# Kernel optimization log

Hardware: AMD Instinct MI355X
Metric: run time of the kernel (lower is better)

## Reference

```python
import jax, jax.numpy as jnp
import numpy as np

GROUP_SIZE = 128
TOP_K = 2
ZERO_POINT = 8  # Marlin symmetric zero point: w = scale * (q - 8)


def _dequant_int4(q, scales, group_size):
    # q: [E, N, K] int values in [0,15]; scales: [E, N, K//group_size]
    s = jnp.repeat(scales, group_size, axis=-1)  # [E, N, K]
    return (q.astype(jnp.float32) - float(ZERO_POINT)) * s


def setup_inputs() -> dict:
    key = jax.random.key(0)
    k1, k2, k3, k4, k5, k6 = jax.random.split(key, 6)
    B, S, H, I, E = 2, 1024, 2048, 1408, 8
    router_logits = jax.random.normal(k1, (B, S, E), dtype=jnp.float32)
    hidden_states = jax.random.normal(k2, (B, S, H), dtype=jnp.float32)
    fc_gate_up_qweights = jax.random.randint(k3, (E, 2 * I, H), 0, 16, dtype=jnp.int32)
    fc_gate_up_scales = jax.random.uniform(k4, (E, 2 * I, H // GROUP_SIZE), dtype=jnp.float32) * 0.02
    fc_down_qweights = jax.random.randint(k5, (E, H, I), 0, 16, dtype=jnp.int32)
    fc_down_scales = jax.random.uniform(k6, (E, H, I // GROUP_SIZE), dtype=jnp.float32) * 0.02
    return {
        "router_logits": router_logits,
        "hidden_states": hidden_states,
        "fc_gate_up_qweights": fc_gate_up_qweights,
        "fc_gate_up_scales": fc_gate_up_scales,
        "fc_down_qweights": fc_down_qweights,
        "fc_down_scales": fc_down_scales,
    }


def reference(router_logits, hidden_states, fc_gate_up_qweights, fc_gate_up_scales,
              fc_down_qweights, fc_down_scales):
    B, S, H = hidden_states.shape
    E = router_logits.shape[-1]
    T = B * S
    x = hidden_states.reshape(T, H)
    logits = router_logits.reshape(T, E)

    # top-k routing with softmax over selected logits
    top_vals, top_idx = jax.lax.top_k(logits, TOP_K)          # [T, k]
    top_w = jax.nn.softmax(top_vals, axis=-1)                 # [T, k]
    route_w = jnp.zeros((T, E), x.dtype).at[jnp.arange(T)[:, None], top_idx].set(top_w)  # [T, E]

    # dequantize int4 weights: scale * (q - 8), per-group along K
    w_gate_up = _dequant_int4(fc_gate_up_qweights, fc_gate_up_scales, GROUP_SIZE)  # [E, 2I, H]
    w_down = _dequant_int4(fc_down_qweights, fc_down_scales, GROUP_SIZE)          # [E, H, I]

    # grouped GEMM (dense over experts, masked by routing weights)
    gu = jnp.einsum('th,enh->ten', x, w_gate_up)              # [T, E, 2I]
    gate, up = jnp.split(gu, 2, axis=-1)
    act = jax.nn.silu(gate) * up                              # SwiGLU, [T, E, I]
    out = jnp.einsum('tei,ehi,te->th', act, w_down, route_w)  # [T, H]
    return out.reshape(B, S, H)
```

## Files before the change

### kernel.cpp

```cpp
#include <hip/hip_runtime.h>
#include <hip/hip_bf16.h>

#define T_TOKENS 2048
#define H_DIM    2048
#define I_DIM    1408
#define E_NUM    8

typedef __bf16 bf16;
typedef __attribute__((ext_vector_type(8))) __bf16  bf16x8;
typedef __attribute__((ext_vector_type(4))) float   floatx4;

static const size_t OFF_COUNTS = 0;
static const size_t OFF_LISTS  = 256;
static const size_t OFF_WLISTS = OFF_LISTS + (size_t)T_TOKENS * E_NUM * 4;
static const size_t OFF_XB     = 131328;
static const size_t OFF_ACT    = OFF_XB + (size_t)T_TOKENS * H_DIM * 2;
static const size_t OFF_GUPK   = OFF_ACT + (size_t)2 * T_TOKENS * I_DIM * 2;
static const size_t OFF_DNPK   = OFF_GUPK + (size_t)E_NUM * 22 * 32 * 16384;
static const size_t OFF_TMP    = OFF_GUPK;

__global__ __launch_bounds__(256) void pack_gu_kernel(const int* __restrict__ q,
                                                      const float* __restrict__ sc,
                                                      bf16* __restrict__ out)
{
    const int b = blockIdx.x;
    const int t = threadIdx.x;
    const int e = b / 2816;
    const int grow = b - e * 2816;
    const int4* qp = reinterpret_cast<const int4*>(q + (size_t)b * H_DIM) + t * 2;
    int4 a = qp[0], c = qp[1];
    float s = sc[(size_t)b * 16 + (t >> 4)];
    float m8s = -8.f * s;
    bf16x8 bv;
    bv[0] = (bf16)fmaf((float)a.x, s, m8s);
    bv[1] = (bf16)fmaf((float)a.y, s, m8s);
    bv[2] = (bf16)fmaf((float)a.z, s, m8s);
    bv[3] = (bf16)fmaf((float)a.w, s, m8s);
    bv[4] = (bf16)fmaf((float)c.x, s, m8s);
    bv[5] = (bf16)fmaf((float)c.y, s, m8s);
    bv[6] = (bf16)fmaf((float)c.z, s, m8s);
    bv[7] = (bf16)fmaf((float)c.w, s, m8s);
    const int is_up = grow >= I_DIM;
    const int icol  = grow - (is_up ? I_DIM : 0);
    const int nt    = icol >> 6;
    const int r     = ((((icol >> 4) & 3) * 2 + is_up) * 16) + (icol & 15);
    size_t dst = ((((size_t)e * 22 + nt) * 32 + (t >> 3)) * 128 + r) * 8 + ((t & 7) ^ (r & 7));
    reinterpret_cast<bf16x8*>(out)[dst] = bv;
}

__global__ __launch_bounds__(256) void pack_dn_kernel(const int* __restrict__ q,
                                                      const float* __restrict__ sc,
                                                      bf16* __restrict__ out)
{
    const int b = blockIdx.x;
    const int t = threadIdx.x;
    if (t >= 176) return;
    const int e = b >> 11;
    const int grow = b & 2047;
    const int4* qp = reinterpret_cast<const int4*>(q + (size_t)b * I_DIM) + t * 2;
    int4 a = qp[0], c = qp[1];
    float s = sc[(size_t)b * 11 + (t >> 4)];
    float m8s = -8.f * s;
    bf16x8 bv;
    bv[0] = (bf16)fmaf((float)a.x, s, m8s);
    bv[1] = (bf16)fmaf((float)a.y, s, m8s);
    bv[2] = (bf16)fmaf((float)a.z, s, m8s);
    bv[3] = (bf16)fmaf((float)a.w, s, m8s);
    bv[4] = (bf16)fmaf((float)c.x, s, m8s);
    bv[5] = (bf16)fmaf((float)c.y, s, m8s);
    bv[6] = (bf16)fmaf((float)c.z, s, m8s);
    bv[7] = (bf16)fmaf((float)c.w, s, m8s);
    const int nt = grow >> 7;
    const int r  = grow & 127;
    size_t dst = ((((size_t)e * 16 + nt) * 22 + (t >> 3)) * 128 + r) * 8 + ((t & 7) ^ (r & 7));
    reinterpret_cast<bf16x8*>(out)[dst] = bv;
}

__global__ void xconv_kernel(const float* __restrict__ x, bf16* __restrict__ xb)
{
    int i = blockIdx.x * blockDim.x + threadIdx.x;
    const float4* x4 = reinterpret_cast<const float4*>(x) + (size_t)i * 2;
    float4 v0 = x4[0], v1 = x4[1];
    bf16x8 bv;
    bv[0] = (bf16)v0.x; bv[1] = (bf16)v0.y; bv[2] = (bf16)v0.z; bv[3] = (bf16)v0.w;
    bv[4] = (bf16)v1.x; bv[5] = (bf16)v1.y; bv[6] = (bf16)v1.z; bv[7] = (bf16)v1.w;
    *reinterpret_cast<bf16x8*>(xb + (size_t)i * 8) = bv;
}

__global__ void router_kernel(const float* __restrict__ logits,
                              int* __restrict__ counts,
                              int* __restrict__ lists,
                              float* __restrict__ wlists)
{
    int t = blockIdx.x * blockDim.x + threadIdx.x;
    if (t >= T_TOKENS) return;
    const float* l = logits + (size_t)t * E_NUM;
    float v0 = -1e30f, v1 = -1e30f;
    int i0 = 0, i1 = 0;
    #pragma unroll
    for (int e = 0; e < E_NUM; ++e) {
        float v = l[e];
        if (v > v0) { v1 = v0; i1 = i0; v0 = v; i0 = e; }
        else if (v > v1) { v1 = v; i1 = e; }
    }
    float w0 = 1.f / (1.f + __expf(v1 - v0));
    float w1 = 1.f - w0;
    int p0 = atomicAdd(&counts[i0], 1);
    lists[i0 * T_TOKENS + p0] = t * 2 + 0;
    wlists[i0 * T_TOKENS + p0] = w0;
    int p1 = atomicAdd(&counts[i1], 1);
    lists[i1 * T_TOKENS + p1] = t * 2 + 1;
    wlists[i1 * T_TOKENS + p1] = w1;
}

__global__ __launch_bounds__(256) void gemm1_kernel(
    const bf16* __restrict__ xb,
    const bf16* __restrict__ wpk,
    const int*  __restrict__ counts,
    const int*  __restrict__ lists,
    bf16*       __restrict__ act)
{
    const int e   = blockIdx.z;
    const int cnt = counts[e];
    const int m0  = blockIdx.y * 128;
    if (m0 >= cnt) return;
    const int nt  = blockIdx.x;

    __shared__ __align__(16) bf16 Al[8192];
    __shared__ __align__(16) bf16 Bl[8192];
    __shared__ int meta[128];

    const int tid = threadIdx.x;
    if (tid < 128) {
        int m = m0 + tid;
        meta[tid] = lists[e * T_TOKENS + (m < cnt ? m : 0)];
    }
    __syncthreads();

    const int lane = tid & 63;
    const int wv = tid >> 6;
    const int wm = wv >> 1, wn = wv & 1;

    int    aoff[4];
    size_t agbl[4];
    #pragma unroll
    for (int j = 0; j < 4; ++j) {
        int g = tid + 256 * j;
        int arow = g >> 3, cg = g & 7;
        aoff[j] = arow * 64 + ((cg ^ (arow & 7)) * 8);
        agbl[j] = (size_t)(meta[arow] >> 1) * H_DIM + cg * 8;
    }
    const bf16* bt = wpk + ((size_t)e * 22 + nt) * (32 * 8192) + tid * 8;

    int afr[2][4], bfr[2][4];
    #pragma unroll
    for (int ks = 0; ks < 2; ++ks) {
        int gidx = ks * 4 + (lane >> 4);
        #pragma unroll
        for (int t4 = 0; t4 < 4; ++t4) {
            int ra = wm * 64 + t4 * 16 + (lane & 15);
            afr[ks][t4] = ra * 64 + ((gidx ^ (ra & 7)) * 8);
            int rb = wn * 64 + t4 * 16 + (lane & 15);
            bfr[ks][t4] = rb * 64 + ((gidx ^ (rb & 7)) * 8);
        }
    }

    floatx4 acc[4][4];
    #pragma unroll
    for (int i = 0; i < 4; ++i)
        #pragma unroll
        for (int j = 0; j < 4; ++j)
            acc[i][j] = (floatx4){0.f, 0.f, 0.f, 0.f};

    for (int k0 = 0; k0 < H_DIM; k0 += 64) {
        #pragma unroll
        for (int j = 0; j < 4; ++j) {
            bf16x8 v = *reinterpret_cast<const bf16x8*>(xb + agbl[j] + k0);
            *reinterpret_cast<bf16x8*>(&Al[aoff[j]]) = v;
        }
        const bf16* bsrc = bt + (size_t)(k0 >> 6) * 8192;
        #pragma unroll
        for (int j = 0; j < 4; ++j) {
            bf16x8 v = *reinterpret_cast<const bf16x8*>(bsrc + j * 2048);
            *reinterpret_cast<bf16x8*>(&Bl[tid * 8 + j * 2048]) = v;
        }
        __syncthreads();
        #pragma unroll
        for (int ks = 0; ks < 2; ++ks) {
            bf16x8 af[4], bff[4];
            #pragma unroll
            for (int mt = 0; mt < 4; ++mt)
                af[mt] = *reinterpret_cast<const bf16x8*>(&Al[afr[ks][mt]]);
            #pragma unroll
            for (int ntf = 0; ntf < 4; ++ntf)
                bff[ntf] = *reinterpret_cast<const bf16x8*>(&Bl[bfr[ks][ntf]]);
            #pragma unroll
            for (int mt = 0; mt < 4; ++mt)
                #pragma unroll
                for (int ntf = 0; ntf < 4; ++ntf)
                    acc[mt][ntf] = __builtin_amdgcn_mfma_f32_16x16x32_bf16(af[mt], bff[ntf], acc[mt][ntf], 0, 0, 0);
        }
        __syncthreads();
    }

    const int rbase = (lane >> 4) * 4;
    const int cn = lane & 15;
    #pragma unroll
    for (int mt = 0; mt < 4; ++mt) {
        #pragma unroll
        for (int j = 0; j < 2; ++j) {
            floatx4 g = acc[mt][2 * j];
            floatx4 u = acc[mt][2 * j + 1];
            int col = nt * 64 + (wn * 2 + j) * 16 + cn;
            #pragma unroll
            for (int r = 0; r < 4; ++r) {
                int lrow = wm * 64 + mt * 16 + rbase + r;
                if (m0 + lrow < cnt) {
                    float gate = g[r], up = u[r];
                    float a = gate / (1.f + __expf(-gate)) * up;
                    act[(size_t)meta[lrow] * I_DIM + col] = (bf16)a;
                }
            }
        }
    }
}

__global__ __launch_bounds__(256) void gemm2_kernel(
    const bf16*  __restrict__ act,
    const bf16*  __restrict__ wpk,
    const int*   __restrict__ counts,
    const int*   __restrict__ lists,
    const float* __restrict__ wlists,
    float*       __restrict__ tmp)
{
    const int e   = blockIdx.z;
    const int cnt = counts[e];
    const int m0  = blockIdx.y * 128;
    if (m0 >= cnt) return;
    const int nt  = blockIdx.x;

    __shared__ __align__(16) bf16 Al[8192];
    __shared__ __align__(16) bf16 Bl[8192];
    __shared__ int   meta[128];
    __shared__ float wmeta[128];

    const int tid = threadIdx.x;
    if (tid < 128) {
        int m = m0 + tid;
        int mm = (m < cnt) ? m : 0;
        meta[tid]  = lists[e * T_TOKENS + mm];
        wmeta[tid] = wlists[e * T_TOKENS + mm];
    }
    __syncthreads();

    const int lane = tid & 63;
    const int wv = tid >> 6;
    const int wm = wv >> 1, wn = wv & 1;

    int    aoff[4];
    size_t agbl[4];
    #pragma unroll
    for (int j = 0; j < 4; ++j) {
        int g = tid + 256 * j;
        int arow = g >> 3, cg = g & 7;
        aoff[j] = arow * 64 + ((cg ^ (arow & 7)) * 8);
        agbl[j] = (size_t)meta[arow] * I_DIM + cg * 8;
    }
    const bf16* bt = wpk + ((size_t)e * 16 + nt) * (22 * 8192) + tid * 8;

    int afr[2][4], bfr[2][4];
    #pragma unroll
    for (int ks = 0; ks < 2; ++ks) {
        int gidx = ks * 4 + (lane >> 4);
        #pragma unroll
        for (int t4 = 0; t4 < 4; ++t4) {
            int ra = wm * 64 + t4 * 16 + (lane & 15);
            afr[ks][t4] = ra * 64 + ((gidx ^ (ra & 7)) * 8);
            int rb = wn * 64 + t4 * 16 + (lane & 15);
            bfr[ks][t4] = rb * 64 + ((gidx ^ (rb & 7)) * 8);
        }
    }

    floatx4 acc[4][4];
    #pragma unroll
    for (int i = 0; i < 4; ++i)
        #pragma unroll
        for (int j = 0; j < 4; ++j)
            acc[i][j] = (floatx4){0.f, 0.f, 0.f, 0.f};

    for (int kt = 0; kt < 22; ++kt) {
        #pragma unroll
        for (int j = 0; j < 4; ++j) {
            bf16x8 v = *reinterpret_cast<const bf16x8*>(act + agbl[j] + kt * 64);
            *reinterpret_cast<bf16x8*>(&Al[aoff[j]]) = v;
        }
        const bf16* bsrc = bt + (size_t)kt * 8192;
        #pragma unroll
        for (int j = 0; j < 4; ++j) {
            bf16x8 v = *reinterpret_cast<const bf16x8*>(bsrc + j * 2048);
            *reinterpret_cast<bf16x8*>(&Bl[tid * 8 + j * 2048]) = v;
        }
        __syncthreads();
        #pragma unroll
        for (int ks = 0; ks < 2; ++ks) {
            bf16x8 af[4], bff[4];
            #pragma unroll
            for (int mt = 0; mt < 4; ++mt)
                af[mt] = *reinterpret_cast<const bf16x8*>(&Al[afr[ks][mt]]);
            #pragma unroll
            for (int ntf = 0; ntf < 4; ++ntf)
                bff[ntf] = *reinterpret_cast<const bf16x8*>(&Bl[bfr[ks][ntf]]);
            #pragma unroll
            for (int mt = 0; mt < 4; ++mt)
                #pragma unroll
                for (int ntf = 0; ntf < 4; ++ntf)
                    acc[mt][ntf] = __builtin_amdgcn_mfma_f32_16x16x32_bf16(af[mt], bff[ntf], acc[mt][ntf], 0, 0, 0);
        }
        __syncthreads();
    }

    const int rbase = (lane >> 4) * 4;
    const int cn = lane & 15;
    #pragma unroll
    for (int mt = 0; mt < 4; ++mt) {
        #pragma unroll
        for (int ntf = 0; ntf < 4; ++ntf) {
            floatx4 v = acc[mt][ntf];
            int col = nt * 128 + wn * 64 + ntf * 16 + cn;
            #pragma unroll
            for (int r = 0; r < 4; ++r) {
                int lrow = wm * 64 + mt * 16 + rbase + r;
                if (m0 + lrow < cnt) {
                    tmp[(size_t)meta[lrow] * H_DIM + col] = wmeta[lrow] * v[r];
                }
            }
        }
    }
}

__global__ void finalize_kernel(const float* __restrict__ tmp, float* __restrict__ out)
{
    int i4 = blockIdx.x * blockDim.x + threadIdx.x;
    int t  = i4 >> 9;
    int h  = (i4 & 511) * 4;
    float4 a = *reinterpret_cast<const float4*>(tmp + ((size_t)2 * t) * H_DIM + h);
    float4 b = *reinterpret_cast<const float4*>(tmp + ((size_t)(2 * t + 1)) * H_DIM + h);
    float4 o;
    o.x = a.x + b.x; o.y = a.y + b.y; o.z = a.z + b.z; o.w = a.w + b.w;
    *reinterpret_cast<float4*>(out + (size_t)t * H_DIM + h) = o;
}

extern "C" void kernel_launch(void* const* d_in, const int* in_sizes, int n_in,
                              void* d_out, int out_size, void* d_ws, size_t ws_size,
                              hipStream_t stream)
{
    const float* router_logits = (const float*)d_in[0];
    const float* x             = (const float*)d_in[1];
    const int*   gu_q          = (const int*)d_in[2];
    const float* gu_s          = (const float*)d_in[3];
    const int*   dn_q          = (const int*)d_in[4];
    const float* dn_s          = (const float*)d_in[5];
    float* out = (float*)d_out;

    char* ws = (char*)d_ws;
    int*   counts = (int*)(ws + OFF_COUNTS);
    int*   lists  = (int*)(ws + OFF_LISTS);
    float* wlists = (float*)(ws + OFF_WLISTS);
    bf16*  xb     = (bf16*)(ws + OFF_XB);
    bf16*  act    = (bf16*)(ws + OFF_ACT);
    bf16*  gu_pk  = (bf16*)(ws + OFF_GUPK);
    bf16*  dn_pk  = (bf16*)(ws + OFF_DNPK);
    float* tmp    = (float*)(ws + OFF_TMP);

    hipMemsetAsync(counts, 0, E_NUM * sizeof(int), stream);

    pack_gu_kernel<<<E_NUM * 2816, 256, 0, stream>>>(gu_q, gu_s, gu_pk);
    pack_dn_kernel<<<E_NUM * 2048, 256, 0, stream>>>(dn_q, dn_s, dn_pk);
    xconv_kernel<<<T_TOKENS * H_DIM / 8 / 256, 256, 0, stream>>>(x, xb);
    router_kernel<<<T_TOKENS / 256, 256, 0, stream>>>(router_logits, counts, lists, wlists);

    gemm1_kernel<<<dim3(22, 16, 8), 256, 0, stream>>>(xb, gu_pk, counts, lists, act);
    gemm2_kernel<<<dim3(16, 16, 8), 256, 0, stream>>>(act, dn_pk, counts, lists, wlists, tmp);
    finalize_kernel<<<4096, 256, 0, stream>>>(tmp, out);
}
```

Measured before the change: 523.4 us.

## Use direct global-to-LDS loads, XCD-aware block remap, and atomic output accumulation

```diff
diff --git a/kernel.cpp b/kernel.cpp
--- a/kernel.cpp
+++ b/kernel.cpp
@@ -17,7 +17,13 @@
 static const size_t OFF_ACT    = OFF_XB + (size_t)T_TOKENS * H_DIM * 2;
 static const size_t OFF_GUPK   = OFF_ACT + (size_t)2 * T_TOKENS * I_DIM * 2;
 static const size_t OFF_DNPK   = OFF_GUPK + (size_t)E_NUM * 22 * 32 * 16384;
-static const size_t OFF_TMP    = OFF_GUPK;
+
+__device__ __forceinline__ void gload_lds16(const bf16* g, bf16* l)
+{
+    __builtin_amdgcn_global_load_lds((const __attribute__((address_space(1))) void*)g,
+                                     (__attribute__((address_space(3))) void*)l,
+                                     16, 0, 0);
+}
 
 __global__ __launch_bounds__(256) void pack_gu_kernel(const int* __restrict__ q,
                                                       const float* __restrict__ sc,
@@ -120,11 +126,13 @@
     const int*  __restrict__ lists,
     bf16*       __restrict__ act)
 {
-    const int e   = blockIdx.z;
+    const int lid = (blockIdx.x & 7) * 352 + (blockIdx.x >> 3);
+    const int e   = lid / 352;
+    const int r_  = lid - e * 352;
+    const int nt  = r_ >> 4;
+    const int m0  = (r_ & 15) * 128;
     const int cnt = counts[e];
-    const int m0  = blockIdx.y * 128;
     if (m0 >= cnt) return;
-    const int nt  = blockIdx.x;
 
     __shared__ __align__(16) bf16 Al[8192];
     __shared__ __align__(16) bf16 Bl[8192];
@@ -141,14 +149,12 @@
     const int wv = tid >> 6;
     const int wm = wv >> 1, wn = wv & 1;
 
-    int    aoff[4];
     size_t agbl[4];
     #pragma unroll
     for (int j = 0; j < 4; ++j) {
         int g = tid + 256 * j;
         int arow = g >> 3, cg = g & 7;
-        aoff[j] = arow * 64 + ((cg ^ (arow & 7)) * 8);
-        agbl[j] = (size_t)(meta[arow] >> 1) * H_DIM + cg * 8;
+        agbl[j] = (size_t)(meta[arow] >> 1) * H_DIM + ((cg ^ (arow & 7)) * 8);
     }
     const bf16* bt = wpk + ((size_t)e * 22 + nt) * (32 * 8192) + tid * 8;
 
@@ -174,16 +180,12 @@
 
     for (int k0 = 0; k0 < H_DIM; k0 += 64) {
         #pragma unroll
-        for (int j = 0; j < 4; ++j) {
-            bf16x8 v = *reinterpret_cast<const bf16x8*>(xb + agbl[j] + k0);
-            *reinterpret_cast<bf16x8*>(&Al[aoff[j]]) = v;
-        }
+        for (int j = 0; j < 4; ++j)
+            gload_lds16(xb + agbl[j] + k0, &Al[(tid + 256 * j) * 8]);
         const bf16* bsrc = bt + (size_t)(k0 >> 6) * 8192;
         #pragma unroll
-        for (int j = 0; j < 4; ++j) {
-            bf16x8 v = *reinterpret_cast<const bf16x8*>(bsrc + j * 2048);
-            *reinterpret_cast<bf16x8*>(&Bl[tid * 8 + j * 2048]) = v;
-        }
+        for (int j = 0; j < 4; ++j)
+            gload_lds16(bsrc + j * 2048, &Bl[tid * 8 + j * 2048]);
         __syncthreads();
         #pragma unroll
         for (int ks = 0; ks < 2; ++ks) {
@@ -231,13 +233,15 @@
     const int*   __restrict__ counts,
     const int*   __restrict__ lists,
     const float* __restrict__ wlists,
-    float*       __restrict__ tmp)
-{
-    const int e   = blockIdx.z;
+    float*       __restrict__ out)
+{
+    const int lid = (blockIdx.x & 7) * 256 + (blockIdx.x >> 3);
+    const int e   = lid >> 8;
+    const int r_  = lid & 255;
+    const int nt  = r_ >> 4;
+    const int m0  = (r_ & 15) * 128;
     const int cnt = counts[e];
-    const int m0  = blockIdx.y * 128;
     if (m0 >= cnt) return;
-    const int nt  = blockIdx.x;
 
     __shared__ __align__(16) bf16 Al[8192];
     __shared__ __align__(16) bf16 Bl[8192];
@@ -257,14 +261,12 @@
     const int wv = tid >> 6;
     const int wm = wv >> 1, wn = wv & 1;
 
-    int    aoff[4];
     size_t agbl[4];
     #pragma unroll
     for (int j = 0; j < 4; ++j) {
         int g = tid + 256 * j;
         int arow = g >> 3, cg = g & 7;
-        aoff[j] = arow * 64 + ((cg ^ (arow & 7)) * 8);
-        agbl[j] = (size_t)meta[arow] * I_DIM + cg * 8;
+        agbl[j] = (size_t)meta[arow] * I_DIM + ((cg ^ (arow & 7)) * 8);
     }
     const bf16* bt = wpk + ((size_t)e * 16 + nt) * (22 * 8192) + tid * 8;
 
@@ -290,16 +292,12 @@
 
     for (int kt = 0; kt < 22; ++kt) {
         #pragma unroll
-        for (int j = 0; j < 4; ++j) {
-            bf16x8 v = *reinterpret_cast<const bf16x8*>(act + agbl[j] + kt * 64);
-            *reinterpret_cast<bf16x8*>(&Al[aoff[j]]) = v;
-        }
+        for (int j = 0; j < 4; ++j)
+            gload_lds16(act + agbl[j] + kt * 64, &Al[(tid + 256 * j) * 8]);
         const bf16* bsrc = bt + (size_t)kt * 8192;
         #pragma unroll
-        for (int j = 0; j < 4; ++j) {
-            bf16x8 v = *reinterpret_cast<const bf16x8*>(bsrc + j * 2048);
-            *reinterpret_cast<bf16x8*>(&Bl[tid * 8 + j * 2048]) = v;
-        }
+        for (int j = 0; j < 4; ++j)
+            gload_lds16(bsrc + j * 2048, &Bl[tid * 8 + j * 2048]);
         __syncthreads();
         #pragma unroll
         for (int ks = 0; ks < 2; ++ks) {
@@ -331,23 +329,12 @@
             for (int r = 0; r < 4; ++r) {
                 int lrow = wm * 64 + mt * 16 + rbase + r;
                 if (m0 + lrow < cnt) {
-                    tmp[(size_t)meta[lrow] * H_DIM + col] = wmeta[lrow] * v[r];
+                    int tok = meta[lrow] >> 1;
+                    atomicAdd(&out[(size_t)tok * H_DIM + col], wmeta[lrow] * v[r]);
                 }
             }
         }
     }
-}
-
-__global__ void finalize_kernel(const float* __restrict__ tmp, float* __restrict__ out)
-{
-    int i4 = blockIdx.x * blockDim.x + threadIdx.x;
-    int t  = i4 >> 9;
-    int h  = (i4 & 511) * 4;
-    float4 a = *reinterpret_cast<const float4*>(tmp + ((size_t)2 * t) * H_DIM + h);
-    float4 b = *reinterpret_cast<const float4*>(tmp + ((size_t)(2 * t + 1)) * H_DIM + h);
-    float4 o;
-    o.x = a.x + b.x; o.y = a.y + b.y; o.z = a.z + b.z; o.w = a.w + b.w;
-    *reinterpret_cast<float4*>(out + (size_t)t * H_DIM + h) = o;
 }
 
 extern "C" void kernel_launch(void* const* d_in, const int* in_sizes, int n_in,
@@ -370,16 +357,15 @@
     bf16*  act    = (bf16*)(ws + OFF_ACT);
     bf16*  gu_pk  = (bf16*)(ws + OFF_GUPK);
     bf16*  dn_pk  = (bf16*)(ws + OFF_DNPK);
-    float* tmp    = (float*)(ws + OFF_TMP);
 
     hipMemsetAsync(counts, 0, E_NUM * sizeof(int), stream);
+    hipMemsetAsync(out, 0, (size_t)T_TOKENS * H_DIM * sizeof(float), stream);
 
     pack_gu_kernel<<<E_NUM * 2816, 256, 0, stream>>>(gu_q, gu_s, gu_pk);
     pack_dn_kernel<<<E_NUM * 2048, 256, 0, stream>>>(dn_q, dn_s, dn_pk);
     xconv_kernel<<<T_TOKENS * H_DIM / 8 / 256, 256, 0, stream>>>(x, xb);
     router_kernel<<<T_TOKENS / 256, 256, 0, stream>>>(router_logits, counts, lists, wlists);
 
-    gemm1_kernel<<<dim3(22, 16, 8), 256, 0, stream>>>(xb, gu_pk, counts, lists, act);
-    gemm2_kernel<<<dim3(16, 16, 8), 256, 0, stream>>>(act, dn_pk, counts, lists, wlists, tmp);
-    finalize_kernel<<<4096, 256, 0, stream>>>(tmp, out);
-}
+    gemm1_kernel<<<22 * 16 * E_NUM, 256, 0, stream>>>(xb, gu_pk, counts, lists, act);
+    gemm2_kernel<<<16 * 16 * E_NUM, 256, 0, stream>>>(act, dn_pk, counts, lists, wlists, out);
+}
```

Result: slower. 544.4 us (+4.0%).

## Use 256x256 tiles with double-buffered direct global-to-LDS loads in MoE GEMMs

Applied to the files above, without the earlier changes.

```diff
diff --git a/kernel.cpp b/kernel.cpp
--- a/kernel.cpp
+++ b/kernel.cpp
@@ -9,6 +9,8 @@
 typedef __bf16 bf16;
 typedef __attribute__((ext_vector_type(8))) __bf16  bf16x8;
 typedef __attribute__((ext_vector_type(4))) float   floatx4;
+
+#define MFMA __builtin_amdgcn_mfma_f32_16x16x32_bf16
 
 static const size_t OFF_COUNTS = 0;
 static const size_t OFF_LISTS  = 256;
@@ -16,8 +18,15 @@
 static const size_t OFF_XB     = 131328;
 static const size_t OFF_ACT    = OFF_XB + (size_t)T_TOKENS * H_DIM * 2;
 static const size_t OFF_GUPK   = OFF_ACT + (size_t)2 * T_TOKENS * I_DIM * 2;
-static const size_t OFF_DNPK   = OFF_GUPK + (size_t)E_NUM * 22 * 32 * 16384;
+static const size_t OFF_DNPK   = OFF_GUPK + (size_t)E_NUM * 11 * 32 * 32768;
 static const size_t OFF_TMP    = OFF_GUPK;
+
+__device__ __forceinline__ void gload_lds16(const bf16* g, bf16* l)
+{
+    __builtin_amdgcn_global_load_lds((const __attribute__((address_space(1))) void*)g,
+                                     (__attribute__((address_space(3))) void*)l,
+                                     16, 0, 0);
+}
 
 __global__ __launch_bounds__(256) void pack_gu_kernel(const int* __restrict__ q,
                                                       const float* __restrict__ sc,
@@ -42,9 +51,9 @@
     bv[7] = (bf16)fmaf((float)c.w, s, m8s);
     const int is_up = grow >= I_DIM;
     const int icol  = grow - (is_up ? I_DIM : 0);
-    const int nt    = icol >> 6;
-    const int r     = ((((icol >> 4) & 3) * 2 + is_up) * 16) + (icol & 15);
-    size_t dst = ((((size_t)e * 22 + nt) * 32 + (t >> 3)) * 128 + r) * 8 + ((t & 7) ^ (r & 7));
+    const int nt    = icol >> 7;
+    const int r     = ((((icol >> 4) & 7) * 2 + is_up) << 4) + (icol & 15);
+    size_t dst = ((((size_t)e * 11 + nt) * 32 + (t >> 3)) * 256 + r) * 8 + ((t & 7) ^ (r & 7));
     reinterpret_cast<bf16x8*>(out)[dst] = bv;
 }
 
@@ -70,9 +79,9 @@
     bv[5] = (bf16)fmaf((float)c.y, s, m8s);
     bv[6] = (bf16)fmaf((float)c.z, s, m8s);
     bv[7] = (bf16)fmaf((float)c.w, s, m8s);
-    const int nt = grow >> 7;
-    const int r  = grow & 127;
-    size_t dst = ((((size_t)e * 16 + nt) * 22 + (t >> 3)) * 128 + r) * 8 + ((t & 7) ^ (r & 7));
+    const int nt = grow >> 8;
+    const int r  = grow & 255;
+    size_t dst = ((((size_t)e * 8 + nt) * 22 + (t >> 3)) * 256 + r) * 8 + ((t & 7) ^ (r & 7));
     reinterpret_cast<bf16x8*>(out)[dst] = bv;
 }
 
@@ -113,119 +122,181 @@
     wlists[i1 * T_TOKENS + p1] = w1;
 }
 
-__global__ __launch_bounds__(256) void gemm1_kernel(
+
+#define PHASE_BAR() do { __builtin_amdgcn_sched_barrier(0); \
+                         __builtin_amdgcn_s_barrier(); \
+                         __builtin_amdgcn_sched_barrier(0); } while (0)
+#define LGK0() do { asm volatile("s_waitcnt lgkmcnt(0)" ::: "memory"); \
+                    __builtin_amdgcn_sched_barrier(0); } while (0)
+
+#define RD(buf, row, g8) (*reinterpret_cast<const bf16x8*>(&(buf)[(row) * 64 + (g8)]))
+
+__global__ __launch_bounds__(512, 2) void gemm1_kernel(
     const bf16* __restrict__ xb,
     const bf16* __restrict__ wpk,
     const int*  __restrict__ counts,
     const int*  __restrict__ lists,
     bf16*       __restrict__ act)
 {
-    const int e   = blockIdx.z;
+    const int bid = blockIdx.x;
+    const int e   = bid / 88;
+    const int r_  = bid - e * 88;
+    const int nt  = r_ >> 3;
+    const int m0  = (r_ & 7) << 8;
     const int cnt = counts[e];
-    const int m0  = blockIdx.y * 128;
     if (m0 >= cnt) return;
-    const int nt  = blockIdx.x;
-
-    __shared__ __align__(16) bf16 Al[8192];
-    __shared__ __align__(16) bf16 Bl[8192];
-    __shared__ int meta[128];
+
+    __shared__ __align__(16) bf16 Al[2][16384];
+    __shared__ __align__(16) bf16 Bl[2][16384];
+    __shared__ int meta[256];
 
     const int tid = threadIdx.x;
-    if (tid < 128) {
+    if (tid < 256) {
         int m = m0 + tid;
         meta[tid] = lists[e * T_TOKENS + (m < cnt ? m : 0)];
     }
     __syncthreads();
 
     const int lane = tid & 63;
-    const int wv = tid >> 6;
-    const int wm = wv >> 1, wn = wv & 1;
-
-    int    aoff[4];
-    size_t agbl[4];
-    #pragma unroll
-    for (int j = 0; j < 4; ++j) {
-        int g = tid + 256 * j;
-        int arow = g >> 3, cg = g & 7;
-        aoff[j] = arow * 64 + ((cg ^ (arow & 7)) * 8);
-        agbl[j] = (size_t)(meta[arow] >> 1) * H_DIM + cg * 8;
-    }
-    const bf16* bt = wpk + ((size_t)e * 22 + nt) * (32 * 8192) + tid * 8;
-
-    int afr[2][4], bfr[2][4];
-    #pragma unroll
-    for (int ks = 0; ks < 2; ++ks) {
-        int gidx = ks * 4 + (lane >> 4);
-        #pragma unroll
-        for (int t4 = 0; t4 < 4; ++t4) {
-            int ra = wm * 64 + t4 * 16 + (lane & 15);
-            afr[ks][t4] = ra * 64 + ((gidx ^ (ra & 7)) * 8);
-            int rb = wn * 64 + t4 * 16 + (lane & 15);
-            bfr[ks][t4] = rb * 64 + ((gidx ^ (rb & 7)) * 8);
-        }
-    }
-
-    floatx4 acc[4][4];
-    #pragma unroll
-    for (int i = 0; i < 4; ++i)
+    const int wm = (tid >> 6) >> 2;
+    const int wn = (tid >> 6) & 3;
+
+    const int cgp = (((tid & 7) ^ ((tid >> 3) & 7)) << 3);
+    size_t aglb[4];
+    #pragma unroll
+    for (int j = 0; j < 4; ++j)
+        aglb[j] = (size_t)(meta[j * 64 + (tid >> 3)] >> 1) * H_DIM + cgp;
+    const bf16* bt = wpk + ((size_t)e * 11 + nt) * (32 * 16384) + (size_t)tid * 8;
+    const int dst8 = tid * 8;
+
+    floatx4 acc[8][4];
+    #pragma unroll
+    for (int i = 0; i < 8; ++i)
         #pragma unroll
         for (int j = 0; j < 4; ++j)
             acc[i][j] = (floatx4){0.f, 0.f, 0.f, 0.f};
 
-    for (int k0 = 0; k0 < H_DIM; k0 += 64) {
-        #pragma unroll
-        for (int j = 0; j < 4; ++j) {
-            bf16x8 v = *reinterpret_cast<const bf16x8*>(xb + agbl[j] + k0);
-            *reinterpret_cast<bf16x8*>(&Al[aoff[j]]) = v;
-        }
-        const bf16* bsrc = bt + (size_t)(k0 >> 6) * 8192;
-        #pragma unroll
-        for (int j = 0; j < 4; ++j) {
-            bf16x8 v = *reinterpret_cast<const bf16x8*>(bsrc + j * 2048);
-            *reinterpret_cast<bf16x8*>(&Bl[tid * 8 + j * 2048]) = v;
-        }
-        __syncthreads();
-        #pragma unroll
-        for (int ks = 0; ks < 2; ++ks) {
-            bf16x8 af[4], bff[4];
-            #pragma unroll
-            for (int mt = 0; mt < 4; ++mt)
-                af[mt] = *reinterpret_cast<const bf16x8*>(&Al[afr[ks][mt]]);
-            #pragma unroll
-            for (int ntf = 0; ntf < 4; ++ntf)
-                bff[ntf] = *reinterpret_cast<const bf16x8*>(&Bl[bfr[ks][ntf]]);
-            #pragma unroll
-            for (int mt = 0; mt < 4; ++mt)
-                #pragma unroll
-                for (int ntf = 0; ntf < 4; ++ntf)
-                    acc[mt][ntf] = __builtin_amdgcn_mfma_f32_16x16x32_bf16(af[mt], bff[ntf], acc[mt][ntf], 0, 0, 0);
-        }
-        __syncthreads();
+    #pragma unroll
+    for (int j = 0; j < 4; ++j) gload_lds16(xb + aglb[j],            &Al[0][dst8 + j * 4096]);
+    #pragma unroll
+    for (int j = 0; j < 4; ++j) gload_lds16(bt + j * 4096,           &Bl[0][dst8 + j * 4096]);
+    #pragma unroll
+    for (int j = 0; j < 4; ++j) gload_lds16(xb + aglb[j] + 64,       &Al[1][dst8 + j * 4096]);
+    #pragma unroll
+    for (int j = 0; j < 4; ++j) gload_lds16(bt + 16384 + j * 4096,   &Bl[1][dst8 + j * 4096]);
+
+    const int l15   = lane & 15;
+    const int g80   = (((lane >> 4) ^ (lane & 7)) << 3);
+    const int g81   = g80 ^ 32;
+    const int abase = wm * 128 + l15;
+    const int bbase = wn * 64 + l15;
+
+    for (int kt = 0; kt < 32; ++kt) {
+        bf16* Ab = Al[kt & 1];
+        bf16* Bb = Bl[kt & 1];
+        if (kt == 31) { asm volatile("s_waitcnt vmcnt(0)" ::: "memory"); }
+        else          { asm volatile("s_waitcnt vmcnt(8)" ::: "memory"); }
+        PHASE_BAR();
+
+        bf16x8 a[4][2], b0[2][2], b1[2][2];
+        #pragma unroll
+        for (int mt = 0; mt < 4; ++mt) {
+            a[mt][0] = RD(Ab, abase + mt * 16, g80);
+            a[mt][1] = RD(Ab, abase + mt * 16, g81);
+        }
+        #pragma unroll
+        for (int nf = 0; nf < 2; ++nf) {
+            b0[nf][0] = RD(Bb, bbase + nf * 16, g80);
+            b0[nf][1] = RD(Bb, bbase + nf * 16, g81);
+        }
+        LGK0();
+        __builtin_amdgcn_s_setprio(1);
+        #pragma unroll
+        for (int ks = 0; ks < 2; ++ks)
+            #pragma unroll
+            for (int mt = 0; mt < 4; ++mt)
+                #pragma unroll
+                for (int nf = 0; nf < 2; ++nf)
+                    acc[mt][nf] = MFMA(a[mt][ks], b0[nf][ks], acc[mt][nf], 0, 0, 0);
+        __builtin_amdgcn_s_setprio(0);
+        PHASE_BAR();
+
+        #pragma unroll
+        for (int nf = 0; nf < 2; ++nf) {
+            b1[nf][0] = RD(Bb, bbase + 32 + nf * 16, g80);
+            b1[nf][1] = RD(Bb, bbase + 32 + nf * 16, g81);
+        }
+        LGK0();
+        __builtin_amdgcn_s_setprio(1);
+        #pragma unroll
+        for (int ks = 0; ks < 2; ++ks)
+            #pragma unroll
+            for (int mt = 0; mt < 4; ++mt)
+                #pragma unroll
+                for (int nf = 0; nf < 2; ++nf)
+                    acc[mt][2 + nf] = MFMA(a[mt][ks], b1[nf][ks], acc[mt][2 + nf], 0, 0, 0);
+        __builtin_amdgcn_s_setprio(0);
+        PHASE_BAR();
+
+        #pragma unroll
+        for (int mt = 0; mt < 4; ++mt) {
+            a[mt][0] = RD(Ab, abase + 64 + mt * 16, g80);
+            a[mt][1] = RD(Ab, abase + 64 + mt * 16, g81);
+        }
+        LGK0();
+        __builtin_amdgcn_s_setprio(1);
+        #pragma unroll
+        for (int ks = 0; ks < 2; ++ks)
+            #pragma unroll
+            for (int mt = 0; mt < 4; ++mt)
+                #pragma unroll
+                for (int nf = 0; nf < 2; ++nf)
+                    acc[4 + mt][2 + nf] = MFMA(a[mt][ks], b1[nf][ks], acc[4 + mt][2 + nf], 0, 0, 0);
+        __builtin_amdgcn_s_setprio(0);
+        PHASE_BAR();
+
+        if (kt < 30) {
+            #pragma unroll
+            for (int j = 0; j < 4; ++j)
+                gload_lds16(xb + aglb[j] + (size_t)(kt + 2) * 64, &Ab[dst8 + j * 4096]);
+            #pragma unroll
+            for (int j = 0; j < 4; ++j)
+                gload_lds16(bt + (size_t)(kt + 2) * 16384 + j * 4096, &Bb[dst8 + j * 4096]);
+        }
+        __builtin_amdgcn_s_setprio(1);
+        #pragma unroll
+        for (int ks = 0; ks < 2; ++ks)
+            #pragma unroll
+            for (int mt = 0; mt < 4; ++mt)
+                #pragma unroll
+                for (int nf = 0; nf < 2; ++nf)
+                    acc[4 + mt][nf] = MFMA(a[mt][ks], b0[nf][ks], acc[4 + mt][nf], 0, 0, 0);
+        __builtin_amdgcn_s_setprio(0);
     }
 
     const int rbase = (lane >> 4) * 4;
     const int cn = lane & 15;
     #pragma unroll
-    for (int mt = 0; mt < 4; ++mt) {
-        #pragma unroll
-        for (int j = 0; j < 2; ++j) {
-            floatx4 g = acc[mt][2 * j];
-            floatx4 u = acc[mt][2 * j + 1];
-            int col = nt * 64 + (wn * 2 + j) * 16 + cn;
+    for (int mt = 0; mt < 8; ++mt) {
+        #pragma unroll
+        for (int q = 0; q < 2; ++q) {
+            floatx4 g = acc[mt][2 * q];
+            floatx4 u = acc[mt][2 * q + 1];
+            int col = nt * 128 + (wn * 2 + q) * 16 + cn;
             #pragma unroll
             for (int r = 0; r < 4; ++r) {
-                int lrow = wm * 64 + mt * 16 + rbase + r;
+                int lrow = wm * 128 + mt * 16 + rbase + r;
                 if (m0 + lrow < cnt) {
                     float gate = g[r], up = u[r];
-                    float a = gate / (1.f + __expf(-gate)) * up;
-                    act[(size_t)meta[lrow] * I_DIM + col] = (bf16)a;
+                    float av = gate / (1.f + __expf(-gate)) * up;
+                    act[(size_t)meta[lrow] * I_DIM + col] = (bf16)av;
                 }
             }
         }
     }
 }
 
-__global__ __launch_bounds__(256) void gemm2_kernel(
+__global__ __launch_bounds__(512, 2) void gemm2_kernel(
     const bf16*  __restrict__ act,
     const bf16*  __restrict__ wpk,
     const int*   __restrict__ counts,
@@ -233,19 +304,21 @@
     const float* __restrict__ wlists,
     float*       __restrict__ tmp)
 {
-    const int e   = blockIdx.z;
+    const int bid = blockIdx.x;
+    const int e   = bid >> 6;
+    const int r_  = bid & 63;
+    const int nt  = r_ >> 3;
+    const int m0  = (r_ & 7) << 8;
     const int cnt = counts[e];
-    const int m0  = blockIdx.y * 128;
     if (m0 >= cnt) return;
-    const int nt  = blockIdx.x;
-
-    __shared__ __align__(16) bf16 Al[8192];
-    __shared__ __align__(16) bf16 Bl[8192];
-    __shared__ int   meta[128];
-    __shared__ float wmeta[128];
+
+    __shared__ __align__(16) bf16 Al[2][16384];
+    __shared__ __align__(16) bf16 Bl[2][16384];
+    __shared__ int   meta[256];
+    __shared__ float wmeta[256];
 
     const int tid = threadIdx.x;
-    if (tid < 128) {
+    if (tid < 256) {
         int m = m0 + tid;
         int mm = (m < cnt) ? m : 0;
         meta[tid]  = lists[e * T_TOKENS + mm];
@@ -254,82 +327,133 @@
     __syncthreads();
 
     const int lane = tid & 63;
-    const int wv = tid >> 6;
-    const int wm = wv >> 1, wn = wv & 1;
-
-    int    aoff[4];
-    size_t agbl[4];
-    #pragma unroll
-    for (int j = 0; j < 4; ++j) {
-        int g = tid + 256 * j;
-        int arow = g >> 3, cg = g & 7;
-        aoff[j] = arow * 64 + ((cg ^ (arow & 7)) * 8);
-        agbl[j] = (size_t)meta[arow] * I_DIM + cg * 8;
-    }
-    const bf16* bt = wpk + ((size_t)e * 16 + nt) * (22 * 8192) + tid * 8;
-
-    int afr[2][4], bfr[2][4];
-    #pragma unroll
-    for (int ks = 0; ks < 2; ++ks) {
-        int gidx = ks * 4 + (lane >> 4);
-        #pragma unroll
-        for (int t4 = 0; t4 < 4; ++t4) {
-            int ra = wm * 64 + t4 * 16 + (lane & 15);
-            afr[ks][t4] = ra * 64 + ((gidx ^ (ra & 7)) * 8);
-            int rb = wn * 64 + t4 * 16 + (lane & 15);
-            bfr[ks][t4] = rb * 64 + ((gidx ^ (rb & 7)) * 8);
-        }
-    }
-
-    floatx4 acc[4][4];
-    #pragma unroll
-    for (int i = 0; i < 4; ++i)
+    const int wm = (tid >> 6) >> 2;
+    const int wn = (tid >> 6) & 3;
+
+    const int cgp = (((tid & 7) ^ ((tid >> 3) & 7)) << 3);
+    size_t aglb[4];
+    #pragma unroll
+    for (int j = 0; j < 4; ++j)
+        aglb[j] = (size_t)meta[j * 64 + (tid >> 3)] * I_DIM + cgp;
+    const bf16* bt = wpk + ((size_t)e * 8 + nt) * (22 * 16384) + (size_t)tid * 8;
+    const int dst8 = tid * 8;
+
+    floatx4 acc[8][4];
+    #pragma unroll
+    for (int i = 0; i < 8; ++i)
         #pragma unroll
         for (int j = 0; j < 4; ++j)
             acc[i][j] = (floatx4){0.f, 0.f, 0.f, 0.f};
 
+    #pragma unroll
+    for (int j = 0; j < 4; ++j) gload_lds16(act + aglb[j],           &Al[0][dst8 + j * 4096]);
+    #pragma unroll
+    for (int j = 0; j < 4; ++j) gload_lds16(bt + j * 4096,           &Bl[0][dst8 + j * 4096]);
+    #pragma unroll
+    for (int j = 0; j < 4; ++j) gload_lds16(act + aglb[j] + 64,      &Al[1][dst8 + j * 4096]);
+    #pragma unroll
+    for (int j = 0; j < 4; ++j) gload_lds16(bt + 16384 + j * 4096,   &Bl[1][dst8 + j * 4096]);
+
+    const int l15   = lane & 15;
+    const int g80   = (((lane >> 4) ^ (lane & 7)) << 3);
+    const int g81   = g80 ^ 32;
+    const int abase = wm * 128 + l15;
+    const int bbase = wn * 64 + l15;
+
     for (int kt = 0; kt < 22; ++kt) {
-        #pragma unroll
-        for (int j = 0; j < 4; ++j) {
-            bf16x8 v = *reinterpret_cast<const bf16x8*>(act + agbl[j] + kt * 64);
-            *reinterpret_cast<bf16x8*>(&Al[aoff[j]]) = v;
-        }
-        const bf16* bsrc = bt + (size_t)kt * 8192;
-        #pragma unroll
-        for (int j = 0; j < 4; ++j) {
-            bf16x8 v = *reinterpret_cast<const bf16x8*>(bsrc + j * 2048);
-            *reinterpret_cast<bf16x8*>(&Bl[tid * 8 + j * 2048]) = v;
-        }
-        __syncthreads();
-        #pragma unroll
-        for (int ks = 0; ks < 2; ++ks) {
-            bf16x8 af[4], bff[4];
-            #pragma unroll
-            for (int mt = 0; mt < 4; ++mt)
-                af[mt] = *reinterpret_cast<const bf16x8*>(&Al[afr[ks][mt]]);
-            #pragma unroll
-            for (int ntf = 0; ntf < 4; ++ntf)
-                bff[ntf] = *reinterpret_cast<const bf16x8*>(&Bl[bfr[ks][ntf]]);
-            #pragma unroll
-            for (int mt = 0; mt < 4; ++mt)
-                #pragma unroll
-                for (int ntf = 0; ntf < 4; ++ntf)
-                    acc[mt][ntf] = __builtin_amdgcn_mfma_f32_16x16x32_bf16(af[mt], bff[ntf], acc[mt][ntf], 0, 0, 0);
-        }
-        __syncthreads();
+        bf16* Ab = Al[kt & 1];
+        bf16* Bb = Bl[kt & 1];
+        if (kt == 21) { asm volatile("s_waitcnt vmcnt(0)" ::: "memory"); }
+        else          { asm volatile("s_waitcnt vmcnt(8)" ::: "memory"); }
+        PHASE_BAR();
+
+        bf16x8 a[4][2], b0[2][2], b1[2][2];
+        #pragma unroll
+        for (int mt = 0; mt < 4; ++mt) {
+            a[mt][0] = RD(Ab, abase + mt * 16, g80);
+            a[mt][1] = RD(Ab, abase + mt * 16, g81);
+        }
+        #pragma unroll
+        for (int nf = 0; nf < 2; ++nf) {
+            b0[nf][0] = RD(Bb, bbase + nf * 16, g80);
+            b0[nf][1] = RD(Bb, bbase + nf * 16, g81);
+        }
+        LGK0();
+        __builtin_amdgcn_s_setprio(1);
+        #pragma unroll
+        for (int ks = 0; ks < 2; ++ks)
+            #pragma unroll
+            for (int mt = 0; mt < 4; ++mt)
+                #pragma unroll
+                for (int nf = 0; nf < 2; ++nf)
+                    acc[mt][nf] = MFMA(a[mt][ks], b0[nf][ks], acc[mt][nf], 0, 0, 0);
+        __builtin_amdgcn_s_setprio(0);
+        PHASE_BAR();
+
+        #pragma unroll
+        for (int nf = 0; nf < 2; ++nf) {
+            b1[nf][0] = RD(Bb, bbase + 32 + nf * 16, g80);
+            b1[nf][1] = RD(Bb, bbase + 32 + nf * 16, g81);
+        }
+        LGK0();
+        __builtin_amdgcn_s_setprio(1);
+        #pragma unroll
+        for (int ks = 0; ks < 2; ++ks)
+            #pragma unroll
+            for (int mt = 0; mt < 4; ++mt)
+                #pragma unroll
+                for (int nf = 0; nf < 2; ++nf)
+                    acc[mt][2 + nf] = MFMA(a[mt][ks], b1[nf][ks], acc[mt][2 + nf], 0, 0, 0);
+        __builtin_amdgcn_s_setprio(0);
+        PHASE_BAR();
+
+        #pragma unroll
+        for (int mt = 0; mt < 4; ++mt) {
+            a[mt][0] = RD(Ab, abase + 64 + mt * 16, g80);
+            a[mt][1] = RD(Ab, abase + 64 + mt * 16, g81);
+        }
+        LGK0();
+        __builtin_amdgcn_s_setprio(1);
+        #pragma unroll
+        for (int ks = 0; ks < 2; ++ks)
+            #pragma unroll
+            for (int mt = 0; mt < 4; ++mt)
+                #pragma unroll
+                for (int nf = 0; nf < 2; ++nf)
+                    acc[4 + mt][2 + nf] = MFMA(a[mt][ks], b1[nf][ks], acc[4 + mt][2 + nf], 0, 0, 0);
+        __builtin_amdgcn_s_setprio(0);
+        PHASE_BAR();
+
+        if (kt < 20) {
+            #pragma unroll
+            for (int j = 0; j < 4; ++j)
+                gload_lds16(act + aglb[j] + (size_t)(kt + 2) * 64, &Ab[dst8 + j * 4096]);
+            #pragma unroll
+            for (int j = 0; j < 4; ++j)
+                gload_lds16(bt + (size_t)(kt + 2) * 16384 + j * 4096, &Bb[dst8 + j * 4096]);
+        }
+        __builtin_amdgcn_s_setprio(1);
+        #pragma unroll
+        for (int ks = 0; ks < 2; ++ks)
+            #pragma unroll
+            for (int mt = 0; mt < 4; ++mt)
+                #pragma unroll
+                for (int nf = 0; nf < 2; ++nf)
+                    acc[4 + mt][nf] = MFMA(a[mt][ks], b0[nf][ks], acc[4 + mt][nf], 0, 0, 0);
+        __builtin_amdgcn_s_setprio(0);
     }
 
     const int rbase = (lane >> 4) * 4;
     const int cn = lane & 15;
     #pragma unroll
-    for (int mt = 0; mt < 4; ++mt) {
-        #pragma unroll
-        for (int ntf = 0; ntf < 4; ++ntf) {
-            floatx4 v = acc[mt][ntf];
-            int col = nt * 128 + wn * 64 + ntf * 16 + cn;
+    for (int mt = 0; mt < 8; ++mt) {
+        #pragma unroll
+        for (int f = 0; f < 4; ++f) {
+            floatx4 v = acc[mt][f];
+            int col = (nt << 8) + wn * 64 + f * 16 + cn;
             #pragma unroll
             for (int r = 0; r < 4; ++r) {
-                int lrow = wm * 64 + mt * 16 + rbase + r;
+                int lrow = wm * 128 + mt * 16 + rbase + r;
                 if (m0 + lrow < cnt) {
                     tmp[(size_t)meta[lrow] * H_DIM + col] = wmeta[lrow] * v[r];
                 }
@@ -379,7 +503,7 @@
     xconv_kernel<<<T_TOKENS * H_DIM / 8 / 256, 256, 0, stream>>>(x, xb);
     router_kernel<<<T_TOKENS / 256, 256, 0, stream>>>(router_logits, counts, lists, wlists);
 
-    gemm1_kernel<<<dim3(22, 16, 8), 256, 0, stream>>>(xb, gu_pk, counts, lists, act);
-    gemm2_kernel<<<dim3(16, 16, 8), 256, 0, stream>>>(act, dn_pk, counts, lists, wlists, tmp);
+    gemm1_kernel<<<88 * E_NUM, 512, 0, stream>>>(xb, gu_pk, counts, lists, act);
+    gemm2_kernel<<<64 * E_NUM, 512, 0, stream>>>(act, dn_pk, counts, lists, wlists, tmp);
     finalize_kernel<<<4096, 256, 0, stream>>>(tmp, out);
 }
```

Measured after the change: 693.4 us. 32.5% more time.
